# Kernel tuning notes

Measured on AMD Instinct MI355X. Metric: run time of the kernel, lower is better.

The kernel has to match this reference:

```python
import jax, jax.numpy as jnp
import numpy as np

B, T, K = 32, 512, 48
START_TAG, STOP_TAG = 46, 47


def setup_inputs() -> dict:
    key = jax.random.key(0)
    k1, k2, k3 = jax.random.split(key, 3)
    features = jax.random.normal(k1, (B, T, K, K), dtype=jnp.float32)
    targets = jax.random.randint(k2, (B, T), 0, K * K)  # flattened (from,to) index
    # lengths in [1, T], sorted descending (pack_padded_sequence convention)
    lengths = jnp.sort(jax.random.randint(k3, (B,), 1, T + 1))[::-1]
    return {"features": features, "targets": targets, "lengths": lengths}


def reference(features, targets, lengths):
    b, t_max, k, _ = features.shape
    # gold score: gather flattened target index per (b, t), masked by length
    flat = features.reshape(b, t_max, k * k)
    scores_at_targets = jnp.take_along_axis(flat, targets[:, :, None], axis=2)[:, :, 0]
    valid = jnp.arange(t_max)[None, :] < lengths[:, None]  # [B, T]
    gold_score = jnp.sum(jnp.where(valid, scores_at_targets, jnp.zeros((), features.dtype)))

    # forward (log-partition) recurrence; t=0 initializes from START row (all lengths >= 1)
    init = features[:, 0, START_TAG, :]  # [B, K]

    def step(carry, inp):
        feat_t, t = inp  # feat_t: [B, K, K] (prev_tag, cur_tag)
        cand = jax.nn.logsumexp(feat_t + carry[:, :, None], axis=1)  # [B, K]
        carry = jnp.where((t < lengths)[:, None], cand, carry)
        return carry, None

    feats_rest = jnp.moveaxis(features[:, 1:], 1, 0)  # [T-1, B, K, K]
    ts = jnp.arange(1, t_max)
    final, _ = jax.lax.scan(step, init, (feats_rest, ts))

    all_paths_scores = jnp.sum(final[:, STOP_TAG])
    return (all_paths_scores - gold_score) / b
```

## Files before the change

### kernel.cpp

```cpp
#include <hip/hip_runtime.h>

#define BB 32
#define TT 512
#define KK 48
#define KK2 2304
#define START_TAG 46
#define STOP_TAG 47
#define L2E 1.4426950408889634f
#define LN2 0.6931471805599453f

typedef int v4i __attribute__((ext_vector_type(4)));

__device__ inline float fast_exp2(float x) {
#if __has_builtin(__builtin_amdgcn_exp2f)
  return __builtin_amdgcn_exp2f(x);
#else
  return exp2f(x);
#endif
}
__device__ inline float fast_log2(float x) {
#if __has_builtin(__builtin_amdgcn_logf)
  return __builtin_amdgcn_logf(x);
#else
  return log2f(x);
#endif
}

template <int CTRL>
__device__ inline float dppf(float v) {
  int i = __float_as_int(v);
  int r = __builtin_amdgcn_update_dpp(i, i, CTRL, 0xF, 0xF, false);
  return __int_as_float(r);
}


#define BL(dst, OFFLIT)                                                      \
  asm volatile("buffer_load_dword %0, %1, %2, 0 offen offset:" OFFLIT        \
               : "=v"(dst) : "v"(voff), "s"(rsrc))
#define LOAD12(P) do {                                                       \
  BL(P##0, "0");    BL(P##1, "192");  BL(P##2, "384");  BL(P##3, "576");     \
  BL(P##4, "768");  BL(P##5, "960");  BL(P##6, "1152"); BL(P##7, "1344");    \
  BL(P##8, "1536"); BL(P##9, "1728"); BL(P##10, "1920"); BL(P##11, "2112");  \
  voff += (unsigned)(KK2 * 4);                                               \
} while (0)

#define STEP(P, TCUR) do {                                                   \
  const int _rd = ((TCUR) - 1) & 1, _wr = (TCUR) & 1;                        \
  float4 _c0 = *(const float4*)&carry_g[_rd][ig * 12 + 0];                   \
  float4 _c1 = *(const float4*)&carry_g[_rd][ig * 12 + 4];                   \
  float4 _c2 = *(const float4*)&carry_g[_rd][ig * 12 + 8];                   \
  asm volatile("s_waitcnt vmcnt(36)" ::: "memory");                          \
  __builtin_amdgcn_sched_barrier(0);                                         \
  float _f0 = fmaf(P##0, L2E, -shift),  _f1 = fmaf(P##1, L2E, -shift);       \
  float _f2 = fmaf(P##2, L2E, -shift),  _f3 = fmaf(P##3, L2E, -shift);       \
  float _f4 = fmaf(P##4, L2E, -shift),  _f5 = fmaf(P##5, L2E, -shift);       \
  float _f6 = fmaf(P##6, L2E, -shift),  _f7 = fmaf(P##7, L2E, -shift);       \
  float _f8 = fmaf(P##8, L2E, -shift),  _f9 = fmaf(P##9, L2E, -shift);       \
  float _f10 = fmaf(P##10, L2E, -shift), _f11 = fmaf(P##11, L2E, -shift);    \
  LOAD12(P); \
  float _y0 = _c0.x + _f0,  _y1 = _c0.y + _f1;                               \
  float _y2 = _c0.z + _f2,  _y3 = _c0.w + _f3;                               \
  float _y4 = _c1.x + _f4,  _y5 = _c1.y + _f5;                               \
  float _y6 = _c1.z + _f6,  _y7 = _c1.w + _f7;                               \
  float _y8 = _c2.x + _f8,  _y9 = _c2.y + _f9;                               \
  float _y10 = _c2.z + _f10, _y11 = _c2.w + _f11;                            \
  float _eA = (fast_exp2(_y0) + fast_exp2(_y1)) +                            \
              (fast_exp2(_y2) + fast_exp2(_y3));                             \
  float _eB = (fast_exp2(_y4) + fast_exp2(_y5)) +                            \
              (fast_exp2(_y6) + fast_exp2(_y7));                             \
  float _eC = (fast_exp2(_y8) + fast_exp2(_y9)) +                            \
              (fast_exp2(_y10) + fast_exp2(_y11));                           \
  float _ss = _eA + _eB + _eC;                                               \
  _ss += dppf<0xB1>(_ss);                                                    \
  _ss += dppf<0x4E>(_ss);                                                    \
  float _mA = fmaxf(fmaxf(_y0, _y1), fmaxf(_y2, _y3));                       \
  float _mB = fmaxf(fmaxf(_y4, _y5), fmaxf(_y6, _y7));                       \
  float _mC = fmaxf(fmaxf(_y8, _y9), fmaxf(_y10, _y11));                     \
  float _mm = fmaxf(fmaxf(_mA, _mB), _mC);                                   \
  _mm = fmaxf(_mm, dppf<0xB1>(_mm));                                         \
  _mm = fmaxf(_mm, dppf<0x4E>(_mm));                                         \
  float _cn = shift + fast_log2(_ss);                                        \
  shift = shift + _mm;                 \
  if (ig == 0) carry_g[_wr][j] = _cn;                                        \
  asm volatile("s_waitcnt lgkmcnt(0)" ::: "memory");                         \
  __builtin_amdgcn_s_barrier();                                              \
} while (0)

__global__ __launch_bounds__(192, 1) void crf_kernel(
    const float* __restrict__ feat,
    const int* __restrict__ targets,
    const int* __restrict__ lengths,
    float* __restrict__ ws,
    float* __restrict__ out) {

  __shared__ float carry_g[2][KK];
  __shared__ float red[4];

  const int b   = blockIdx.x;
  const int len = lengths[b];
  const int tid = threadIdx.x;
  const int w   = tid >> 6;
  const int l   = tid & 63;
  const int j0  = l >> 2;
  const int ig  = l & 3;
  const int j   = w * 16 + j0;
  const float* fb = feat + (size_t)b * TT * KK2;

  float gsum = 0.f;
  for (int t = tid; t < TT; t += 192)
    if (t < len) gsum += fb[(size_t)t * KK2 + targets[b * TT + t]];
  #pragma unroll
  for (int mk = 1; mk < 64; mk <<= 1) gsum += __shfl_xor(gsum, mk, 64);
  if (l == 0) red[w] = gsum;

  if (tid < KK) carry_g[0][tid] = fb[START_TAG * KK + tid] * L2E;
  float shift = fb[START_TAG * KK + j] * L2E;

  __syncthreads();
  const float gold_b = red[0] + red[1] + red[2];

  union { const float* p; unsigned int u[2]; } ba; ba.p = fb;
  v4i rsrc;
  rsrc.x = (int)ba.u[0];
  rsrc.y = (int)(ba.u[1] & 0xFFFFu);
  rsrc.z = (int)((unsigned)(BB - b) * TT * KK2 * 4);
  rsrc.w = 0x00020000;

  unsigned int voff = (unsigned)(KK2 * 4) + (unsigned)(ig * 12 * KK * 4)
                    + (unsigned)(j * 4);

  float pa0,pa1,pa2,pa3,pa4,pa5,pa6,pa7,pa8,pa9,pa10,pa11;
  float pb0,pb1,pb2,pb3,pb4,pb5,pb6,pb7,pb8,pb9,pb10,pb11;
  float pc0,pc1,pc2,pc3,pc4,pc5,pc6,pc7,pc8,pc9,pc10,pc11;
  float pd0,pd1,pd2,pd3,pd4,pd5,pd6,pd7,pd8,pd9,pd10,pd11;
  LOAD12(pa); LOAD12(pb); LOAD12(pc); LOAD12(pd);

  for (int tb = 1; tb < len; tb += 4) {
    { STEP(pa, tb); }
    if (tb + 1 < len) { STEP(pb, tb + 1); }
    if (tb + 2 < len) { STEP(pc, tb + 2); }
    if (tb + 3 < len) { STEP(pd, tb + 3); }
  }
  asm volatile("s_waitcnt vmcnt(0)" ::: "memory");

  if (tid == 0) {
    const int rdf = (len - 1) & 1;
    float v = carry_g[rdf][STOP_TAG] * LN2 - gold_b;
    atomicAdd(&ws[0], v);
    __threadfence();
    int done = atomicAdd((int*)&ws[1], 1);
    if (done == BB - 1) out[0] = atomicAdd(&ws[0], 0.0f) / (float)BB;
  }
}

extern "C" void kernel_launch(void* const* d_in, const int* in_sizes, int n_in,
                              void* d_out, int out_size, void* d_ws, size_t ws_size,
                              hipStream_t stream) {
  const float* feat  = (const float*)d_in[0];
  const int* targets = (const int*)d_in[1];
  const int* lengths = (const int*)d_in[2];
  float* ws  = (float*)d_ws;
  float* out = (float*)d_out;

  hipMemsetAsync(d_ws, 0, 16, stream);
  crf_kernel<<<BB, 192, 0, stream>>>(feat, targets, lengths, ws, out);
}
```

Before: 389.7 us.

## Run CRF forward recurrence in linear space with exponent-based rescaling

Replaces the per-step log-space logsumexp (add shift, exp2, max, log2) with a linear-space matrix-vector product on exp(features) times the carry. Each step takes the exponent of one carry entry as a power-of-two scale, applies it as an exact rescale, and accumulates the exponent in an integer that is added back after a single log2 at the end. This drops the max reduction and the log2 from the serial critical path. In exchange it relies on the exponent clamp and the shared reference entry to avoid overflow and underflow, which may lose precision when tag scores spread widely.

New measurement: 383.5 us. No clear change (-1.6%).

```diff
diff --git a/kernel.cpp b/kernel.cpp
--- a/kernel.cpp
+++ b/kernel.cpp
@@ -46,42 +46,33 @@
 
 #define STEP(P, TCUR) do {                                                   \
   const int _rd = ((TCUR) - 1) & 1, _wr = (TCUR) & 1;                        \
+  float _uref = carry_g[_rd][40];                                            \
   float4 _c0 = *(const float4*)&carry_g[_rd][ig * 12 + 0];                   \
   float4 _c1 = *(const float4*)&carry_g[_rd][ig * 12 + 4];                   \
   float4 _c2 = *(const float4*)&carry_g[_rd][ig * 12 + 8];                   \
   asm volatile("s_waitcnt vmcnt(36)" ::: "memory");                          \
   __builtin_amdgcn_sched_barrier(0);                                         \
-  float _f0 = fmaf(P##0, L2E, -shift),  _f1 = fmaf(P##1, L2E, -shift);       \
-  float _f2 = fmaf(P##2, L2E, -shift),  _f3 = fmaf(P##3, L2E, -shift);       \
-  float _f4 = fmaf(P##4, L2E, -shift),  _f5 = fmaf(P##5, L2E, -shift);       \
-  float _f6 = fmaf(P##6, L2E, -shift),  _f7 = fmaf(P##7, L2E, -shift);       \
-  float _f8 = fmaf(P##8, L2E, -shift),  _f9 = fmaf(P##9, L2E, -shift);       \
-  float _f10 = fmaf(P##10, L2E, -shift), _f11 = fmaf(P##11, L2E, -shift);    \
-  LOAD12(P); \
-  float _y0 = _c0.x + _f0,  _y1 = _c0.y + _f1;                               \
-  float _y2 = _c0.z + _f2,  _y3 = _c0.w + _f3;                               \
-  float _y4 = _c1.x + _f4,  _y5 = _c1.y + _f5;                               \
-  float _y6 = _c1.z + _f6,  _y7 = _c1.w + _f7;                               \
-  float _y8 = _c2.x + _f8,  _y9 = _c2.y + _f9;                               \
-  float _y10 = _c2.z + _f10, _y11 = _c2.w + _f11;                            \
-  float _eA = (fast_exp2(_y0) + fast_exp2(_y1)) +                            \
-              (fast_exp2(_y2) + fast_exp2(_y3));                             \
-  float _eB = (fast_exp2(_y4) + fast_exp2(_y5)) +                            \
-              (fast_exp2(_y6) + fast_exp2(_y7));                             \
-  float _eC = (fast_exp2(_y8) + fast_exp2(_y9)) +                            \
-              (fast_exp2(_y10) + fast_exp2(_y11));                           \
-  float _ss = _eA + _eB + _eC;                                               \
-  _ss += dppf<0xB1>(_ss);                                                    \
-  _ss += dppf<0x4E>(_ss);                                                    \
-  float _mA = fmaxf(fmaxf(_y0, _y1), fmaxf(_y2, _y3));                       \
-  float _mB = fmaxf(fmaxf(_y4, _y5), fmaxf(_y6, _y7));                       \
-  float _mC = fmaxf(fmaxf(_y8, _y9), fmaxf(_y10, _y11));                     \
-  float _mm = fmaxf(fmaxf(_mA, _mB), _mC);                                   \
-  _mm = fmaxf(_mm, dppf<0xB1>(_mm));                                         \
-  _mm = fmaxf(_mm, dppf<0x4E>(_mm));                                         \
-  float _cn = shift + fast_log2(_ss);                                        \
-  shift = shift + _mm;                 \
-  if (ig == 0) carry_g[_wr][j] = _cn;                                        \
+            \
+  float _e0 = fast_exp2(P##0 * L2E),  _e1 = fast_exp2(P##1 * L2E);           \
+  float _e2 = fast_exp2(P##2 * L2E),  _e3 = fast_exp2(P##3 * L2E);           \
+  float _e4 = fast_exp2(P##4 * L2E),  _e5 = fast_exp2(P##5 * L2E);           \
+  float _e6 = fast_exp2(P##6 * L2E),  _e7 = fast_exp2(P##7 * L2E);           \
+  float _e8 = fast_exp2(P##8 * L2E),  _e9 = fast_exp2(P##9 * L2E);           \
+  float _e10 = fast_exp2(P##10 * L2E), _e11 = fast_exp2(P##11 * L2E);        \
+  LOAD12(P);                                   \
+  unsigned _eb = (__float_as_uint(_uref) >> 23) & 0xFFu;                     \
+  _eb = _eb < 64u ? 64u : (_eb > 190u ? 190u : _eb);       \
+  float _scale = __uint_as_float((254u - _eb) << 23);                        \
+  Mi += (int)_eb - 127;                                                      \
+         \
+  float _h0 = fmaf(_c0.z, _e2, fmaf(_c0.y, _e1, _c0.x * _e0));               \
+  float _h1 = fmaf(_c1.y, _e5, fmaf(_c1.x, _e4, _c0.w * _e3));               \
+  float _h2 = fmaf(_c2.x, _e8, fmaf(_c1.w, _e7, _c1.z * _e6));               \
+  float _h3 = fmaf(_c2.w, _e11, fmaf(_c2.z, _e10, _c2.y * _e9));             \
+  float _v = (_h0 + _h1) + (_h2 + _h3);                                      \
+  _v += dppf<0xB1>(_v);                                                      \
+  _v += dppf<0x4E>(_v);                                                      \
+  if (ig == 0) carry_g[_wr][j] = _v * _scale;                                \
   asm volatile("s_waitcnt lgkmcnt(0)" ::: "memory");                         \
   __builtin_amdgcn_s_barrier();                                              \
 } while (0)
@@ -113,8 +104,8 @@
   for (int mk = 1; mk < 64; mk <<= 1) gsum += __shfl_xor(gsum, mk, 64);
   if (l == 0) red[w] = gsum;
 
-  if (tid < KK) carry_g[0][tid] = fb[START_TAG * KK + tid] * L2E;
-  float shift = fb[START_TAG * KK + j] * L2E;
+  if (tid < KK) carry_g[0][tid] = fast_exp2(fb[START_TAG * KK + tid] * L2E);
+  int Mi = 0;
 
   __syncthreads();
   const float gold_b = red[0] + red[1] + red[2];
@@ -145,7 +136,7 @@
 
   if (tid == 0) {
     const int rdf = (len - 1) & 1;
-    float v = carry_g[rdf][STOP_TAG] * LN2 - gold_b;
+    float v = (fast_log2(carry_g[rdf][STOP_TAG]) + (float)Mi) * LN2 - gold_b;
     atomicAdd(&ws[0], v);
     __threadfence();
     int done = atomicAdd((int*)&ws[1], 1);
```
